# Kernel tuning notes

Measured on AMD Instinct MI355X. Metric: run time of the kernel, lower is better.

## Reference

```python
import jax, jax.numpy as jnp
import numpy as np

N_NODES = 100_000
N_EDGES = 1_600_000
N_GRAPHS = 512
NODE_TYPE_BUCKETS = 256
IDENT_BUCKETS = 50_000
NODE_EMB = 64
IDENT_EMB = 32
IN_DIM = NODE_EMB + IDENT_EMB + 6  # 102
HID = 128
NUM_CATS = 10


def setup_inputs() -> dict:
    key = jax.random.key(0)
    ks = jax.random.split(key, 24)
    p = lambda k, shp: (jax.random.normal(k, shp, dtype=jnp.float32) * 0.05)
    return {
        "node_type_ids": jax.random.randint(ks[0], (N_NODES,), 0, NODE_TYPE_BUCKETS + 2),
        "ident_hash_ids": jax.random.randint(ks[1], (N_NODES,), 0, IDENT_BUCKETS + 2),
        "literal_flags": jax.random.uniform(ks[2], (N_NODES, 5), dtype=jnp.float32),
        "node_depth": jax.random.randint(ks[3], (N_NODES,), 0, 60),
        "edge_index": jax.random.randint(ks[4], (2, N_EDGES), 0, N_NODES),
        "batch_index": jnp.sort(jax.random.randint(ks[5], (N_NODES,), 0, N_GRAPHS)),
        "emb_node": p(ks[6], (NODE_TYPE_BUCKETS + 2, NODE_EMB)),
        "emb_ident": p(ks[7], (IDENT_BUCKETS + 2, IDENT_EMB)),
        "W_self0": p(ks[8], (IN_DIM, HID)), "b_self0": p(ks[9], (HID,)),
        "W_neigh0": p(ks[10], (IN_DIM, HID)), "b_neigh0": p(ks[11], (HID,)),
        "W_self1": p(ks[12], (HID, HID)), "b_self1": p(ks[13], (HID,)),
        "W_neigh1": p(ks[14], (HID, HID)), "b_neigh1": p(ks[15], (HID,)),
        "W_risk": p(ks[16], (HID, 1)), "b_risk": p(ks[17], (1,)),
        "W_cat": p(ks[18], (HID, NUM_CATS)), "b_cat": p(ks[19], (NUM_CATS,)),
    }


def reference(node_type_ids, ident_hash_ids, literal_flags, node_depth,
              edge_index, batch_index, emb_node, emb_ident,
              W_self0, b_self0, W_neigh0, b_neigh0,
              W_self1, b_self1, W_neigh1, b_neigh1,
              W_risk, b_risk, W_cat, b_cat):
    n = node_type_ids.shape[0]
    # node features: [N, 64+32+5+1]
    depth = node_depth.astype(jnp.float32)[:, None]
    depth = depth / jnp.maximum(depth.max(), 1.0)
    x = jnp.concatenate([emb_node[node_type_ids], emb_ident[ident_hash_ids],
                         literal_flags, depth], axis=-1)
    src, dst = edge_index[0], edge_index[1]
    # in-degree, shared across layers (clamped to 1)
    deg = jax.ops.segment_sum(jnp.ones_like(dst, jnp.float32), dst, num_segments=n)
    inv_deg = (1.0 / jnp.maximum(deg, 1.0))[:, None]

    def sage(x, Ws, bs, Wn, bn):
        agg = jax.ops.segment_sum(x[src], dst, num_segments=n)  # gather+scatter-sum
        neigh = agg * inv_deg
        return jax.nn.relu(x @ Ws + bs + neigh @ Wn + bn)

    x = sage(x, W_self0, b_self0, W_neigh0, b_neigh0)
    x = sage(x, W_self1, b_self1, W_neigh1, b_neigh1)

    # global mean pool over graphs
    pooled = jax.ops.segment_sum(x, batch_index, num_segments=N_GRAPHS)
    counts = jax.ops.segment_sum(jnp.ones((n,), jnp.float32), batch_index,
                                 num_segments=N_GRAPHS)
    g = pooled / jnp.maximum(counts, 1.0)[:, None]

    risk_logit = (g @ W_risk + b_risk)[:, 0]
    category_logits = g @ W_cat + b_cat
    return risk_logit, category_logits
```

## Files before the change

### kernel.cpp

```cpp
#include <hip/hip_runtime.h>
#include <cstdint>
#include <cstddef>

#define HIDDIM 128
#define NGRAPH_MAX 512
#define LDSPAD 136
#define NBKT_MAX 512


using short8 = __attribute__((ext_vector_type(8))) short;
using f32x4  = __attribute__((ext_vector_type(4))) float;

__device__ __forceinline__ unsigned short f2bf(float x) {
    union { float f; uint32_t u; } v; v.f = x;
    uint32_t r = v.u + 0x7fffu + ((v.u >> 16) & 1u);
    return (unsigned short)(r >> 16);
}
__device__ __forceinline__ uint32_t pack2(float a, float b) {
    return (uint32_t)f2bf(a) | ((uint32_t)f2bf(b) << 16);
}
__device__ __forceinline__ float bflo(uint32_t u) { return __uint_as_float(u << 16); }
__device__ __forceinline__ float bfhi(uint32_t u) { return __uint_as_float(u & 0xffff0000u); }

__global__ void k_prep(const int* __restrict__ nt, const int* __restrict__ ih,
                       const float* __restrict__ flags, const int* __restrict__ depth,
                       const float* __restrict__ embN, const float* __restrict__ embI,
                       const int* __restrict__ edst, const int* __restrict__ batch,
                       const float* __restrict__ Wn0, const float* __restrict__ Ws0,
                       const float* __restrict__ Wn1, const float* __restrict__ Ws1,
                       int K0, int N, int E, int G,
                       unsigned short* __restrict__ x0, unsigned short* __restrict__ Wt,
                       int* __restrict__ bcount, int* __restrict__ counts,
                       int* __restrict__ maxd,
                       int nbF, int nbC, int nbN) {
    __shared__ int hist[NBKT_MAX];
    __shared__ int red[256];
    int b = blockIdx.x, t = threadIdx.x;
    if (b < nbF) {
        int idx = b * 256 + t;
        int i = idx >> 4;
        int seg = idx & 15;
        if (i >= N) return;
        uint4 o = make_uint4(0u, 0u, 0u, 0u);
        if (seg < 8) {
            const float4* r = (const float4*)(embN + (size_t)nt[i] * 64 + seg * 8);
            float4 v0 = r[0], v1 = r[1];
            o.x = pack2(v0.x, v0.y); o.y = pack2(v0.z, v0.w);
            o.z = pack2(v1.x, v1.y); o.w = pack2(v1.z, v1.w);
        } else if (seg < 12) {
            const float4* r = (const float4*)(embI + (size_t)ih[i] * 32 + (seg - 8) * 8);
            float4 v0 = r[0], v1 = r[1];
            o.x = pack2(v0.x, v0.y); o.y = pack2(v0.z, v0.w);
            o.z = pack2(v1.x, v1.y); o.w = pack2(v1.z, v1.w);
        } else if (seg == 12) {
            const float* fp = flags + (size_t)i * 5;
            o.x = pack2(fp[0], fp[1]);
            o.y = pack2(fp[2], fp[3]);
            o.z = pack2(fp[4], 0.f);
        }
        *(uint4*)(x0 + (size_t)i * HIDDIM + seg * 8) = o;
    } else if (b < nbF + nbC) {
        hist[t] = 0; hist[t + 256] = 0;
        __syncthreads();
        int c0 = (b - nbF) * 4096;
        int ce = min(4096, E - c0);
        for (int i = t; i < ce; i += 256)
            atomicAdd(&hist[edst[c0 + i] >> 8], 1);
        __syncthreads();
        for (int bb = t; bb < NBKT_MAX; bb += 256)
            if (hist[bb]) atomicAdd(&bcount[bb], hist[bb]);
    } else if (b < nbF + nbC + nbN) {
        for (int g = t; g < G; g += 256) hist[g] = 0;
        __syncthreads();
        int i = (b - nbF - nbC) * 256 + t;
        int d = 0;
        if (i < N) {
            atomicAdd(&hist[batch[i]], 1);
            d = depth[i];
        }
        red[t] = d;
        __syncthreads();
        for (int off = 128; off > 0; off >>= 1) {
            if (t < off) red[t] = max(red[t], red[t + off]);
            __syncthreads();
        }
        if (t == 0) atomicMax(maxd, red[0]);
        for (int g = t; g < G; g += 256)
            if (hist[g]) atomicAdd(&counts[g], hist[g]);
    } else {
        int idx = (b - nbF - nbC - nbN) * 256 + t;
        int mat = idx >> 14;
        int rem = idx & 16383;
        int n = rem >> 7, k = rem & 127;
        const float* W = (mat == 0) ? Wn0 : (mat == 1) ? Ws0 : (mat == 2) ? Wn1 : Ws1;
        int K = (mat < 2) ? K0 : HIDDIM;
        Wt[(size_t)mat * HIDDIM * HIDDIM + n * HIDDIM + k] =
            (k < K) ? f2bf(W[(size_t)k * HIDDIM + n]) : (unsigned short)0;
    }
}

__global__ void k_scan2x(const int* __restrict__ bcount, int* __restrict__ boff,
                         int* __restrict__ bcur, int* __restrict__ rowptr,
                         const int* __restrict__ counts, int* __restrict__ gstart,
                         const int* __restrict__ depth, const int* __restrict__ maxd,
                         unsigned short* __restrict__ x0,
                         int nbkt, int N, int E, int G) {
    __shared__ int sd[512];
    int b = blockIdx.x, t = threadIdx.x;
    if (b == 0) {
        int v = (t < nbkt) ? bcount[t] : 0;
        sd[t] = v;
        __syncthreads();
        for (int off = 1; off < 512; off <<= 1) {
            int x = (t >= off) ? sd[t - off] : 0;
            __syncthreads();
            sd[t] += x;
            __syncthreads();
        }
        if (t < nbkt) { boff[t] = sd[t] - v; bcur[t] = sd[t] - v; }
        if (t == 0) { boff[nbkt] = E; rowptr[N] = E; }
    } else if (b == 1) {
        int v = (t < G) ? counts[t] : 0;
        sd[t] = v;
        __syncthreads();
        for (int off = 1; off < 512; off <<= 1) {
            int x = (t >= off) ? sd[t - off] : 0;
            __syncthreads();
            sd[t] += x;
            __syncthreads();
        }
        if (t < G) gstart[t] = sd[t] - v;
        if (t == G - 1) gstart[G] = sd[t];
    } else {
        int i = (b - 2) * 512 + t;
        if (i < N) {
            float md = fmaxf((float)(*maxd), 1.0f);
            x0[(size_t)i * HIDDIM + 101] = f2bf((float)depth[i] / md);
        }
    }
}

__global__ void k_bscatter(const int* __restrict__ src, const int* __restrict__ dst,
                           int* __restrict__ bcur, uint32_t* __restrict__ ebuf, int E, int nbkt) {
    __shared__ uint32_t stage[4096];
    __shared__ int hist[NBKT_MAX];
    __shared__ int ofs[NBKT_MAX];
    __shared__ int cur[NBKT_MAX];
    __shared__ int gbase[NBKT_MAX];
    __shared__ int scanbuf[256];
    int t = threadIdx.x;
    int c0 = blockIdx.x * 4096;
    int ce = min(4096, E - c0);

    hist[t] = 0; hist[t + 256] = 0;
    __syncthreads();
    for (int i = t; i < ce; i += 256)
        atomicAdd(&hist[dst[c0 + i] >> 8], 1);
    __syncthreads();
    int h2a = hist[2 * t], h2b = hist[2 * t + 1];
    int ps = h2a + h2b;
    scanbuf[t] = ps;
    __syncthreads();
    for (int off = 1; off < 256; off <<= 1) {
        int x = (t >= off) ? scanbuf[t - off] : 0;
        __syncthreads();
        scanbuf[t] += x;
        __syncthreads();
    }
    int ex = scanbuf[t] - ps;
    ofs[2 * t] = ex;           cur[2 * t] = ex;
    ofs[2 * t + 1] = ex + h2a; cur[2 * t + 1] = ex + h2a;
    __syncthreads();
    for (int i = t; i < ce; i += 256) {
        int d = dst[c0 + i];
        int p = atomicAdd(&cur[d >> 8], 1);
        stage[p] = (uint32_t)src[c0 + i] | ((uint32_t)(d & 255) << 24);
    }
    __syncthreads();
    for (int b = t; b < nbkt; b += 256) {
        int c = hist[b];
        gbase[b] = c ? atomicAdd(&bcur[b], c) : 0;
    }
    __syncthreads();
    for (int j = t; j < ce; j += 256) {
        uint32_t p = stage[j];
        (void)p;
        break;
    }
    __syncthreads();
    for (int b = t; b < nbkt; b += 256) {
        int cnt = hist[b];
        if (!cnt) continue;
        int lo = ofs[b];
        int gb = gbase[b];
        for (int k = 0; k < cnt; k++)
            ebuf[gb + k] = stage[lo + k];
    }
}

__global__ void k_build(const uint32_t* __restrict__ ebuf, const int* __restrict__ boff,
                        int* __restrict__ rowptr, float* __restrict__ invd,
                        int* __restrict__ srcs, int N) {
    __shared__ int ldeg[256];
    __shared__ int lofs[256];
    __shared__ int lcur[256];
    int b = blockIdx.x, t = threadIdx.x;
    int n0 = b << 8;
    int s = boff[b], e = boff[b + 1];
    ldeg[t] = 0;
    __syncthreads();
    for (int i = s + t; i < e; i += 256)
        atomicAdd(&ldeg[ebuf[i] >> 24], 1);
    __syncthreads();
    int v = ldeg[t];
    lofs[t] = v;
    __syncthreads();
    for (int off = 1; off < 256; off <<= 1) {
        int x = (t >= off) ? lofs[t - off] : 0;
        __syncthreads();
        lofs[t] += x;
        __syncthreads();
    }
    int excl = lofs[t] - v;
    int node = n0 + t;
    if (node < N) {
        rowptr[node] = s + excl;
        invd[node] = 1.0f / (float)max(v, 1);
    }
    lcur[t] = excl;
    __syncthreads();
    for (int i = s + t; i < e; i += 256) {
        uint32_t p = ebuf[i];
        int slot = atomicAdd(&lcur[p >> 24], 1);
        srcs[s + slot] = (int)(p & 0x00FFFFFFu);
    }
}

__global__ void k_aggc(const uint4* __restrict__ x4, const int* __restrict__ rp,
                       const int* __restrict__ srcs, const float* __restrict__ invd,
                       uint4* __restrict__ axo, int N) {
    int t = threadIdx.x;
    int lane = t & 63;
    int q = lane >> 4;
    int cl = lane & 15;
    int d = blockIdx.x * 4 + (t >> 6);
    if (d >= N) return;
    int s = rp[d], e = rp[d + 1];
    float a0 = 0.f, a1 = 0.f, a2 = 0.f, a3 = 0.f,
          a4 = 0.f, a5 = 0.f, a6 = 0.f, a7 = 0.f;
#define ACC8(u) { a0 += bflo(u.x); a1 += bfhi(u.x); a2 += bflo(u.y); a3 += bfhi(u.y); \
                  a4 += bflo(u.z); a5 += bfhi(u.z); a6 += bflo(u.w); a7 += bfhi(u.w); }
    for (int base = s; base < e; base += 64) {
        int m = min(64, e - base);
        int idx = (lane < m) ? srcs[base + lane] : 0;
        int j = 0;
        for (; j + 16 <= m; j += 16) {
            int i0 = __shfl(idx, j + q, 64);
            int i1 = __shfl(idx, j + 4 + q, 64);
            int i2 = __shfl(idx, j + 8 + q, 64);
            int i3 = __shfl(idx, j + 12 + q, 64);
            uint4 u0 = x4[(size_t)i0 * 16 + cl];
            uint4 u1 = x4[(size_t)i1 * 16 + cl];
            uint4 u2 = x4[(size_t)i2 * 16 + cl];
            uint4 u3 = x4[(size_t)i3 * 16 + cl];
            ACC8(u0); ACC8(u1); ACC8(u2); ACC8(u3);
        }
        for (; j + 4 <= m; j += 4) {
            int id = __shfl(idx, j + q, 64);
            uint4 u = x4[(size_t)id * 16 + cl];
            ACC8(u);
        }
        if (j < m) {
            int id = __shfl(idx, min(j + q, m - 1), 64);
            if (q < m - j) {
                uint4 u = x4[(size_t)id * 16 + cl];
                ACC8(u);
            }
        }
    }
#undef ACC8
    a0 += __shfl_down(a0, 32, 64); a1 += __shfl_down(a1, 32, 64);
    a2 += __shfl_down(a2, 32, 64); a3 += __shfl_down(a3, 32, 64);
    a4 += __shfl_down(a4, 32, 64); a5 += __shfl_down(a5, 32, 64);
    a6 += __shfl_down(a6, 32, 64); a7 += __shfl_down(a7, 32, 64);
    a0 += __shfl_down(a0, 16, 64); a1 += __shfl_down(a1, 16, 64);
    a2 += __shfl_down(a2, 16, 64); a3 += __shfl_down(a3, 16, 64);
    a4 += __shfl_down(a4, 16, 64); a5 += __shfl_down(a5, 16, 64);
    a6 += __shfl_down(a6, 16, 64); a7 += __shfl_down(a7, 16, 64);
    if (q == 0) {
        float iv = invd[d];
        uint4 o;
        o.x = pack2(a0 * iv, a1 * iv);
        o.y = pack2(a2 * iv, a3 * iv);
        o.z = pack2(a4 * iv, a5 * iv);
        o.w = pack2(a6 * iv, a7 * iv);
        axo[(size_t)d * 16 + cl] = o;
    }
}

__global__ __launch_bounds__(256, 2) void k_gemm3(
    const unsigned short* __restrict__ X, const unsigned short* __restrict__ AX,
    const unsigned short* __restrict__ Wts, const unsigned short* __restrict__ Wtn,
    int N, const float* __restrict__ bias_s, const float* __restrict__ bias_n,
    unsigned short* __restrict__ Xo) {
    __shared__ unsigned short Bs[128 * LDSPAD];
    __shared__ unsigned short Bn[128 * LDSPAD];
    int t = threadIdx.x;
    int rowBase = blockIdx.x << 7;

    #pragma unroll
    for (int it = 0; it < 8; it++) {
        int idx = t + it * 256;
        int n = idx >> 4, seg = idx & 15;
        *(uint4*)&Bs[n * LDSPAD + seg * 8] = *(const uint4*)(Wts + n * HIDDIM + seg * 8);
        *(uint4*)&Bn[n * LDSPAD + seg * 8] = *(const uint4*)(Wtn + n * HIDDIM + seg * 8);
    }

    int lane = t & 63;
    int wv = t >> 6;
    int ml = lane & 15;
    int quad = lane >> 4;
    int m0 = wv * 32;

    const uint4* X4 = (const uint4*)X;
    const uint4* A4 = (const uint4*)AX;
    int gr0 = rowBase + m0 + ml;
    int gr1 = gr0 + 16;
    uint4 fx0[4], fx1[4], fa0[4], fa1[4];
    #pragma unroll
    for (int kt = 0; kt < 4; kt++) {
        uint4 z = make_uint4(0u, 0u, 0u, 0u);
        size_t o0 = (size_t)gr0 * 16 + kt * 4 + quad;
        size_t o1 = (size_t)gr1 * 16 + kt * 4 + quad;
        fx0[kt] = (gr0 < N) ? X4[o0] : z;
        fx1[kt] = (gr1 < N) ? X4[o1] : z;
        fa0[kt] = (gr0 < N) ? A4[o0] : z;
        fa1[kt] = (gr1 < N) ? A4[o1] : z;
    }
    __syncthreads();

    f32x4 acc[2][8];
    #pragma unroll
    for (int i = 0; i < 2; i++)
        #pragma unroll
        for (int j = 0; j < 8; j++) acc[i][j] = (f32x4){0.f, 0.f, 0.f, 0.f};

    #pragma unroll
    for (int kt = 0; kt < 4; kt++) {
        int ko = kt * 32 + quad * 8;
        short8 x0f = *(short8*)&fx0[kt];
        short8 x1f = *(short8*)&fx1[kt];
        short8 a0f = *(short8*)&fa0[kt];
        short8 a1f = *(short8*)&fa1[kt];
        #pragma unroll
        for (int nt = 0; nt < 8; nt++) {
            short8 bs = *(const short8*)&Bs[(nt * 16 + ml) * LDSPAD + ko];
            short8 bn = *(const short8*)&Bn[(nt * 16 + ml) * LDSPAD + ko];
            acc[0][nt] = __builtin_amdgcn_mfma_f32_16x16x32_bf16(x0f, bs, acc[0][nt], 0, 0, 0);
            acc[1][nt] = __builtin_amdgcn_mfma_f32_16x16x32_bf16(x1f, bs, acc[1][nt], 0, 0, 0);
            acc[0][nt] = __builtin_amdgcn_mfma_f32_16x16x32_bf16(a0f, bn, acc[0][nt], 0, 0, 0);
            acc[1][nt] = __builtin_amdgcn_mfma_f32_16x16x32_bf16(a1f, bn, acc[1][nt], 0, 0, 0);
        }
    }

    float bsum[8];
    #pragma unroll
    for (int nt = 0; nt < 8; nt++) {
        int col = nt * 16 + ml;
        bsum[nt] = bias_s[col] + bias_n[col];
    }

    __syncthreads();
    #pragma unroll
    for (int mt = 0; mt < 2; mt++) {
        int lrow0 = m0 + mt * 16 + quad * 4;
        #pragma unroll
        for (int r = 0; r < 4; r++)
            #pragma unroll
            for (int nt = 0; nt < 8; nt++)
                Bs[(lrow0 + r) * LDSPAD + nt * 16 + ml] =
                    f2bf(fmaxf(acc[mt][nt][r] + bsum[nt], 0.f));
    }
    __syncthreads();
    #pragma unroll
    for (int it = 0; it < 8; it++) {
        int idx = t + it * 256;
        int r = idx >> 4, seg = idx & 15;
        int gr = rowBase + r;
        if (gr < N)
            *(uint4*)(Xo + (size_t)gr * HIDDIM + seg * 8) = *(const uint4*)&Bs[r * LDSPAD + seg * 8];
    }
}

__global__ void k_poolhead(const uint32_t* __restrict__ x, const int* __restrict__ gstart,
                           const int* __restrict__ counts,
                           const float* __restrict__ Wr, const float* __restrict__ br,
                           const float* __restrict__ Wc, const float* __restrict__ bc,
                           float* __restrict__ out, int G) {
    __shared__ float red[3][128];
    __shared__ float rowf[128];
    int gr = blockIdx.x, t = threadIdx.x;
    int wv = t >> 6, lane = t & 63;
    int half = lane >> 5, cl = lane & 31;
    int s = gstart[gr], e = gstart[gr + 1];
    const uint2* x2 = (const uint2*)x;
    float a0 = 0.f, a1 = 0.f, a2 = 0.f, a3 = 0.f;
    for (int r0 = s + wv * 2 + half; r0 < e; r0 += 32) {
        uint2 u0 = x2[(size_t)r0 * 32 + cl];
        int r1 = r0 + 8, r2 = r0 + 16, r3 = r0 + 24;
        uint2 u1 = make_uint2(0u, 0u), u2 = make_uint2(0u, 0u), u3 = make_uint2(0u, 0u);
        if (r1 < e) u1 = x2[(size_t)r1 * 32 + cl];
        if (r2 < e) u2 = x2[(size_t)r2 * 32 + cl];
        if (r3 < e) u3 = x2[(size_t)r3 * 32 + cl];
        a0 += bflo(u0.x); a1 += bfhi(u0.x); a2 += bflo(u0.y); a3 += bfhi(u0.y);
        a0 += bflo(u1.x); a1 += bfhi(u1.x); a2 += bflo(u1.y); a3 += bfhi(u1.y);
        a0 += bflo(u2.x); a1 += bfhi(u2.x); a2 += bflo(u2.y); a3 += bfhi(u2.y);
        a0 += bflo(u3.x); a1 += bfhi(u3.x); a2 += bflo(u3.y); a3 += bfhi(u3.y);
    }
    a0 += __shfl_down(a0, 32, 64);
    a1 += __shfl_down(a1, 32, 64);
    a2 += __shfl_down(a2, 32, 64);
    a3 += __shfl_down(a3, 32, 64);
    if (half == 0 && wv > 0) {
        red[wv - 1][cl * 4 + 0] = a0;
        red[wv - 1][cl * 4 + 1] = a1;
        red[wv - 1][cl * 4 + 2] = a2;
        red[wv - 1][cl * 4 + 3] = a3;
    }
    __syncthreads();
    if (wv == 0 && half == 0) {
        a0 += red[0][cl * 4 + 0] + red[1][cl * 4 + 0] + red[2][cl * 4 + 0];
        a1 += red[0][cl * 4 + 1] + red[1][cl * 4 + 1] + red[2][cl * 4 + 1];
        a2 += red[0][cl * 4 + 2] + red[1][cl * 4 + 2] + red[2][cl * 4 + 2];
        a3 += red[0][cl * 4 + 3] + red[1][cl * 4 + 3] + red[2][cl * 4 + 3];
        float inv = 1.0f / fmaxf((float)counts[gr], 1.0f);
        rowf[cl * 4 + 0] = a0 * inv;
        rowf[cl * 4 + 1] = a1 * inv;
        rowf[cl * 4 + 2] = a2 * inv;
        rowf[cl * 4 + 3] = a3 * inv;
    }
    __syncthreads();
    if (t == 0) {
        float s2 = 0.f;
        for (int k = 0; k < 128; k++) s2 += rowf[k] * Wr[k];
        out[gr] = s2 + br[0];
    } else if (t <= 10) {
        int j = t - 1;
        float s2 = 0.f;
        for (int k = 0; k < 128; k++) s2 += rowf[k] * Wc[k * 10 + j];
        out[G + gr * 10 + j] = s2 + bc[j];
    }
}

extern "C" void kernel_launch(void* const* d_in, const int* in_sizes, int n_in,
                              void* d_out, int out_size, void* d_ws, size_t ws_size,
                              hipStream_t stream) {
    const int*   nt    = (const int*)d_in[0];
    const int*   ih    = (const int*)d_in[1];
    const float* flags = (const float*)d_in[2];
    const int*   depth = (const int*)d_in[3];
    const int*   eidx  = (const int*)d_in[4];
    const int*   batch = (const int*)d_in[5];
    const float* embN  = (const float*)d_in[6];
    const float* embI  = (const float*)d_in[7];
    const float* Ws0   = (const float*)d_in[8];
    const float* bs0   = (const float*)d_in[9];
    const float* Wn0   = (const float*)d_in[10];
    const float* bn0   = (const float*)d_in[11];
    const float* Ws1   = (const float*)d_in[12];
    const float* bs1   = (const float*)d_in[13];
    const float* Wn1   = (const float*)d_in[14];
    const float* bn1   = (const float*)d_in[15];
    const float* Wr    = (const float*)d_in[16];
    const float* br    = (const float*)d_in[17];
    const float* Wc    = (const float*)d_in[18];
    const float* bc    = (const float*)d_in[19];
    float* out = (float*)d_out;

    const int N  = in_sizes[0];
    const int E  = in_sizes[4] / 2;
    const int K0 = in_sizes[8] / HIDDIM;
    const int G  = out_size / 11;
    const int* esrc = eidx;
    const int* edst = eidx + E;
    const int NBKT = (N + 255) >> 8;

    char* w = (char*)d_ws;
    const size_t NH = (size_t)N * HIDDIM * sizeof(unsigned short);
    unsigned short* bufA  = (unsigned short*)(w);
    unsigned short* bufB  = (unsigned short*)(w + NH);
    unsigned short* bufAX = (unsigned short*)(w + 2 * NH);
    char* p = w + 3 * NH;
    unsigned short* Wt = (unsigned short*)p; p += (size_t)4 * HIDDIM * HIDDIM * 2;
    uint32_t* ebuf = (uint32_t*)p;   p += (size_t)E * 4;
    int* srcs   = (int*)p;           p += (size_t)E * 4;
    int* rowptr = (int*)p;           p += (size_t)(N + 1) * 4;
    float* invd = (float*)p;         p += (size_t)N * 4;
    int* gstart = (int*)p;           p += (size_t)(G + 1) * 4;
    int* boff   = (int*)p;           p += (size_t)(NBKT_MAX + 1) * 4;
    int* bcur   = (int*)p;           p += (size_t)NBKT_MAX * 4;
    int* bcount = (int*)p;           p += (size_t)NBKT_MAX * 4;
    int* counts = (int*)p;           p += (size_t)G * 4;
    int* maxd   = (int*)p;           p += 4;
    const size_t zero_bytes = (size_t)(NBKT_MAX + G + 1) * 4;
    (void)n_in; (void)ws_size;

    const int nbC = (E + 4095) / 4096;
    const int nbN = (N + 255) / 256;
    const int nbF = ((size_t)N * 16 + 255) / 256;
    const int nbG2 = (N + 127) / 128;
    const int nbA = (N + 3) / 4;
    const int nbD = (N + 511) / 512;

    hipMemsetAsync(bcount, 0, zero_bytes, stream);

    k_prep<<<nbF + nbC + nbN + 256, 256, 0, stream>>>(
        nt, ih, flags, depth, embN, embI, edst, batch,
        Wn0, Ws0, Wn1, Ws1, K0, N, E, G,
        bufA, Wt, bcount, counts, maxd, nbF, nbC, nbN);

    k_scan2x<<<2 + nbD, 512, 0, stream>>>(bcount, boff, bcur, rowptr,
                                          counts, gstart, depth, maxd, bufA,
                                          NBKT, N, E, G);

    k_bscatter<<<nbC, 256, 0, stream>>>(esrc, edst, bcur, ebuf, E, NBKT);
    k_build<<<NBKT, 256, 0, stream>>>(ebuf, boff, rowptr, invd, srcs, N);

    const unsigned short* Wt_n0 = Wt;
    const unsigned short* Wt_s0 = Wt + 1 * HIDDIM * HIDDIM;
    const unsigned short* Wt_n1 = Wt + 2 * HIDDIM * HIDDIM;
    const unsigned short* Wt_s1 = Wt + 3 * HIDDIM * HIDDIM;

    k_aggc<<<nbA, 256, 0, stream>>>((const uint4*)bufA, rowptr, srcs, invd,
                                    (uint4*)bufAX, N);
    k_gemm3<<<nbG2, 256, 0, stream>>>(bufA, bufAX, Wt_s0, Wt_n0, N, bs0, bn0, bufB);

    k_aggc<<<nbA, 256, 0, stream>>>((const uint4*)bufB, rowptr, srcs, invd,
                                    (uint4*)bufAX, N);
    k_gemm3<<<nbG2, 256, 0, stream>>>(bufB, bufAX, Wt_s1, Wt_n1, N, bs1, bn1, bufA);

    k_poolhead<<<G, 256, 0, stream>>>((const uint32_t*)bufA, gstart, counts,
                                      Wr, br, Wc, bc, out, G);
}
```

Measured before the change: 342.5 us.

## Fuse CSR scan, bucket scatter and build into one cooperative kernel

Merges three separate CSR-construction kernels (bucket/graph scans plus depth write, edge bucket scatter, per-bucket build) into a single cooperative launch that uses grid-wide syncs between phases. The goal is to remove two kernel launch gaps and their tail effects. It also replaces the serial per-bucket copy loop in the scatter phase with a coalesced copy, where each staged edge records its bucket id in a new LDS array. The trade-off is that a cooperative launch needs every block resident at once: the grid is about 400 blocks, each using roughly 30KB of LDS, and grid.sync itself has a cost.

After: 554.6 us. 61.9% more time.

```diff
diff --git a/kernel.cpp b/kernel.cpp
--- a/kernel.cpp
+++ b/kernel.cpp
@@ -1,4 +1,5 @@
 #include <hip/hip_runtime.h>
+#include <hip/hip_cooperative_groups.h>
 #include <cstdint>
 #include <cstddef>
 
@@ -99,140 +100,141 @@
     }
 }
 
-__global__ void k_scan2x(const int* __restrict__ bcount, int* __restrict__ boff,
-                         int* __restrict__ bcur, int* __restrict__ rowptr,
-                         const int* __restrict__ counts, int* __restrict__ gstart,
-                         const int* __restrict__ depth, const int* __restrict__ maxd,
-                         unsigned short* __restrict__ x0,
-                         int nbkt, int N, int E, int G) {
-    __shared__ int sd[512];
-    int b = blockIdx.x, t = threadIdx.x;
-    if (b == 0) {
-        int v = (t < nbkt) ? bcount[t] : 0;
-        sd[t] = v;
-        __syncthreads();
-        for (int off = 1; off < 512; off <<= 1) {
-            int x = (t >= off) ? sd[t - off] : 0;
-            __syncthreads();
-            sd[t] += x;
-            __syncthreads();
-        }
-        if (t < nbkt) { boff[t] = sd[t] - v; bcur[t] = sd[t] - v; }
-        if (t == 0) { boff[nbkt] = E; rowptr[N] = E; }
-    } else if (b == 1) {
-        int v = (t < G) ? counts[t] : 0;
-        sd[t] = v;
-        __syncthreads();
-        for (int off = 1; off < 512; off <<= 1) {
-            int x = (t >= off) ? sd[t - off] : 0;
-            __syncthreads();
-            sd[t] += x;
-            __syncthreads();
-        }
-        if (t < G) gstart[t] = sd[t] - v;
-        if (t == G - 1) gstart[G] = sd[t];
-    } else {
-        int i = (b - 2) * 512 + t;
-        if (i < N) {
-            float md = fmaxf((float)(*maxd), 1.0f);
-            x0[(size_t)i * HIDDIM + 101] = f2bf((float)depth[i] / md);
-        }
-    }
-}
-
-__global__ void k_bscatter(const int* __restrict__ src, const int* __restrict__ dst,
-                           int* __restrict__ bcur, uint32_t* __restrict__ ebuf, int E, int nbkt) {
+__global__ void k_csr(const int* __restrict__ src, const int* __restrict__ dst,
+                      const int* __restrict__ bcount, int* __restrict__ boff,
+                      int* __restrict__ bcur, int* __restrict__ rowptr,
+                      const int* __restrict__ counts, int* __restrict__ gstart,
+                      const int* __restrict__ depth, const int* __restrict__ maxd,
+                      unsigned short* __restrict__ x0,
+                      uint32_t* __restrict__ ebuf, float* __restrict__ invd,
+                      int* __restrict__ srcs,
+                      int nbkt, int N, int E, int G, int nbC) {
+    cooperative_groups::grid_group grid = cooperative_groups::this_grid();
     __shared__ uint32_t stage[4096];
+    __shared__ unsigned short sbkt[4096];
     __shared__ int hist[NBKT_MAX];
     __shared__ int ofs[NBKT_MAX];
     __shared__ int cur[NBKT_MAX];
     __shared__ int gbase[NBKT_MAX];
     __shared__ int scanbuf[256];
-    int t = threadIdx.x;
-    int c0 = blockIdx.x * 4096;
-    int ce = min(4096, E - c0);
-
-    hist[t] = 0; hist[t + 256] = 0;
-    __syncthreads();
-    for (int i = t; i < ce; i += 256)
-        atomicAdd(&hist[dst[c0 + i] >> 8], 1);
-    __syncthreads();
-    int h2a = hist[2 * t], h2b = hist[2 * t + 1];
-    int ps = h2a + h2b;
-    scanbuf[t] = ps;
-    __syncthreads();
-    for (int off = 1; off < 256; off <<= 1) {
-        int x = (t >= off) ? scanbuf[t - off] : 0;
-        __syncthreads();
-        scanbuf[t] += x;
-        __syncthreads();
-    }
-    int ex = scanbuf[t] - ps;
-    ofs[2 * t] = ex;           cur[2 * t] = ex;
-    ofs[2 * t + 1] = ex + h2a; cur[2 * t + 1] = ex + h2a;
-    __syncthreads();
-    for (int i = t; i < ce; i += 256) {
-        int d = dst[c0 + i];
-        int p = atomicAdd(&cur[d >> 8], 1);
-        stage[p] = (uint32_t)src[c0 + i] | ((uint32_t)(d & 255) << 24);
-    }
-    __syncthreads();
-    for (int b = t; b < nbkt; b += 256) {
-        int c = hist[b];
-        gbase[b] = c ? atomicAdd(&bcur[b], c) : 0;
-    }
-    __syncthreads();
-    for (int j = t; j < ce; j += 256) {
-        uint32_t p = stage[j];
-        (void)p;
-        break;
-    }
-    __syncthreads();
-    for (int b = t; b < nbkt; b += 256) {
-        int cnt = hist[b];
-        if (!cnt) continue;
-        int lo = ofs[b];
-        int gb = gbase[b];
-        for (int k = 0; k < cnt; k++)
-            ebuf[gb + k] = stage[lo + k];
-    }
-}
-
-__global__ void k_build(const uint32_t* __restrict__ ebuf, const int* __restrict__ boff,
-                        int* __restrict__ rowptr, float* __restrict__ invd,
-                        int* __restrict__ srcs, int N) {
-    __shared__ int ldeg[256];
-    __shared__ int lofs[256];
-    __shared__ int lcur[256];
     int b = blockIdx.x, t = threadIdx.x;
-    int n0 = b << 8;
-    int s = boff[b], e = boff[b + 1];
-    ldeg[t] = 0;
-    __syncthreads();
-    for (int i = s + t; i < e; i += 256)
-        atomicAdd(&ldeg[ebuf[i] >> 24], 1);
-    __syncthreads();
-    int v = ldeg[t];
-    lofs[t] = v;
-    __syncthreads();
-    for (int off = 1; off < 256; off <<= 1) {
-        int x = (t >= off) ? lofs[t - off] : 0;
-        __syncthreads();
-        lofs[t] += x;
-        __syncthreads();
-    }
-    int excl = lofs[t] - v;
-    int node = n0 + t;
-    if (node < N) {
-        rowptr[node] = s + excl;
-        invd[node] = 1.0f / (float)max(v, 1);
-    }
-    lcur[t] = excl;
-    __syncthreads();
-    for (int i = s + t; i < e; i += 256) {
-        uint32_t p = ebuf[i];
-        int slot = atomicAdd(&lcur[p >> 24], 1);
-        srcs[s + slot] = (int)(p & 0x00FFFFFFu);
+
+    if (b == 0) {
+        int e0 = 2 * t, e1 = 2 * t + 1;
+        int v0 = (e0 < nbkt) ? bcount[e0] : 0;
+        int v1 = (e1 < nbkt) ? bcount[e1] : 0;
+        int ps = v0 + v1;
+        scanbuf[t] = ps;
+        __syncthreads();
+        for (int off = 1; off < 256; off <<= 1) {
+            int x = (t >= off) ? scanbuf[t - off] : 0;
+            __syncthreads();
+            scanbuf[t] += x;
+            __syncthreads();
+        }
+        int ex = scanbuf[t] - ps;
+        if (e0 < nbkt) { boff[e0] = ex; bcur[e0] = ex; }
+        if (e1 < nbkt) { boff[e1] = ex + v0; bcur[e1] = ex + v0; }
+        if (t == 0) { boff[nbkt] = E; rowptr[N] = E; }
+    } else if (b == 1) {
+        int e0 = 2 * t, e1 = 2 * t + 1;
+        int v0 = (e0 < G) ? counts[e0] : 0;
+        int v1 = (e1 < G) ? counts[e1] : 0;
+        int ps = v0 + v1;
+        scanbuf[t] = ps;
+        __syncthreads();
+        for (int off = 1; off < 256; off <<= 1) {
+            int x = (t >= off) ? scanbuf[t - off] : 0;
+            __syncthreads();
+            scanbuf[t] += x;
+            __syncthreads();
+        }
+        int ex = scanbuf[t] - ps;
+        if (e0 < G) gstart[e0] = ex;
+        if (e1 < G) gstart[e1] = ex + v0;
+        if (t == 255) gstart[G] = scanbuf[255];
+    } else {
+        int i = (b - 2) * 256 + t;
+        if (i < N) {
+            float md = fmaxf((float)(*maxd), 1.0f);
+            x0[(size_t)i * HIDDIM + 101] = f2bf((float)depth[i] / md);
+        }
+    }
+    __threadfence();
+    grid.sync();
+
+    if (b < nbC) {
+        int c0 = b * 4096;
+        int ce = min(4096, E - c0);
+        hist[t] = 0; hist[t + 256] = 0;
+        __syncthreads();
+        for (int i = t; i < ce; i += 256)
+            atomicAdd(&hist[dst[c0 + i] >> 8], 1);
+        __syncthreads();
+        int h2a = hist[2 * t], h2b = hist[2 * t + 1];
+        int ps = h2a + h2b;
+        scanbuf[t] = ps;
+        __syncthreads();
+        for (int off = 1; off < 256; off <<= 1) {
+            int x = (t >= off) ? scanbuf[t - off] : 0;
+            __syncthreads();
+            scanbuf[t] += x;
+            __syncthreads();
+        }
+        int ex = scanbuf[t] - ps;
+        ofs[2 * t] = ex;           cur[2 * t] = ex;
+        ofs[2 * t + 1] = ex + h2a; cur[2 * t + 1] = ex + h2a;
+        __syncthreads();
+        for (int i = t; i < ce; i += 256) {
+            int d = dst[c0 + i];
+            int p = atomicAdd(&cur[d >> 8], 1);
+            stage[p] = (uint32_t)src[c0 + i] | ((uint32_t)(d & 255) << 24);
+            sbkt[p] = (unsigned short)(d >> 8);
+        }
+        __syncthreads();
+        for (int bb = t; bb < nbkt; bb += 256) {
+            int c = hist[bb];
+            gbase[bb] = c ? atomicAdd(&bcur[bb], c) : 0;
+        }
+        __syncthreads();
+        for (int j = t; j < ce; j += 256) {
+            int bk = sbkt[j];
+            ebuf[gbase[bk] + (j - ofs[bk])] = stage[j];
+        }
+    }
+    __threadfence();
+    grid.sync();
+
+    if (b < nbkt) {
+        int n0 = b << 8;
+        int s = boff[b], e = boff[b + 1];
+        hist[t] = 0;
+        __syncthreads();
+        for (int i = s + t; i < e; i += 256)
+            atomicAdd(&hist[ebuf[i] >> 24], 1);
+        __syncthreads();
+        int v = hist[t];
+        ofs[t] = v;
+        __syncthreads();
+        for (int off = 1; off < 256; off <<= 1) {
+            int x = (t >= off) ? ofs[t - off] : 0;
+            __syncthreads();
+            ofs[t] += x;
+            __syncthreads();
+        }
+        int excl = ofs[t] - v;
+        int node = n0 + t;
+        if (node < N) {
+            rowptr[node] = s + excl;
+            invd[node] = 1.0f / (float)max(v, 1);
+        }
+        cur[t] = excl;
+        __syncthreads();
+        for (int i = s + t; i < e; i += 256) {
+            uint32_t p = ebuf[i];
+            int slot = atomicAdd(&cur[p >> 24], 1);
+            srcs[s + slot] = (int)(p & 0x00FFFFFFu);
+        }
     }
 }
 
@@ -510,7 +512,6 @@
     const int nbF = ((size_t)N * 16 + 255) / 256;
     const int nbG2 = (N + 127) / 128;
     const int nbA = (N + 3) / 4;
-    const int nbD = (N + 511) / 512;
 
     hipMemsetAsync(bcount, 0, zero_bytes, stream);
 
@@ -519,12 +520,26 @@
         Wn0, Ws0, Wn1, Ws1, K0, N, E, G,
         bufA, Wt, bcount, counts, maxd, nbF, nbC, nbN);
 
-    k_scan2x<<<2 + nbD, 512, 0, stream>>>(bcount, boff, bcur, rowptr,
-                                          counts, gstart, depth, maxd, bufA,
-                                          NBKT, N, E, G);
-
-    k_bscatter<<<nbC, 256, 0, stream>>>(esrc, edst, bcur, ebuf, E, NBKT);
-    k_build<<<NBKT, 256, 0, stream>>>(ebuf, boff, rowptr, invd, srcs, N);
+    {
+        const int nbD256 = (N + 255) / 256;
+        int nbCoop = nbC;
+        if (NBKT > nbCoop) nbCoop = NBKT;
+        if (2 + nbD256 > nbCoop) nbCoop = 2 + nbD256;
+        const int* a_src = esrc; const int* a_dst = edst;
+        const int* a_bcount = bcount;
+        int* a_boff = boff; int* a_bcur = bcur; int* a_rowptr = rowptr;
+        const int* a_counts = counts; int* a_gstart = gstart;
+        const int* a_depth = depth; const int* a_maxd = maxd;
+        unsigned short* a_x0 = bufA;
+        uint32_t* a_ebuf = ebuf; float* a_invd = invd; int* a_srcs = srcs;
+        int v_nbkt = NBKT, v_N = N, v_E = E, v_G = G, v_nbC = nbC;
+        void* cargs[] = { &a_src, &a_dst, &a_bcount, &a_boff, &a_bcur, &a_rowptr,
+                          &a_counts, &a_gstart, &a_depth, &a_maxd, &a_x0,
+                          &a_ebuf, &a_invd, &a_srcs,
+                          &v_nbkt, &v_N, &v_E, &v_G, &v_nbC };
+        hipLaunchCooperativeKernel((void*)k_csr, dim3(nbCoop), dim3(256),
+                                   cargs, 0, stream);
+    }
 
     const unsigned short* Wt_n0 = Wt;
     const unsigned short* Wt_s0 = Wt + 1 * HIDDIM * HIDDIM;
```
